# Kernel tuning notes

Measured on AMD Instinct MI355X. Metric: run time of the kernel, lower is better.

## Reference

```python
import jax, jax.numpy as jnp
import numpy as np

B, T, C, H = 8, 2048, 1024, 64

def setup_inputs() -> dict:
    key = jax.random.key(0)
    kx, kk, kq, kv = jax.random.split(key, 4)
    x = jax.random.normal(kx, (B, T, C), dtype=jnp.float32)
    # nn.Linear(n_embed, head_size, bias=False) weights stored as [C, H] (already transposed)
    s = 1.0 / np.sqrt(C)
    Wk = jax.random.normal(kk, (C, H), dtype=jnp.float32) * s
    Wq = jax.random.normal(kq, (C, H), dtype=jnp.float32) * s
    Wv = jax.random.normal(kv, (C, H), dtype=jnp.float32) * s
    return {"x": x, "Wk": Wk, "Wq": Wq, "Wv": Wv}

def reference(x, Wk, Wq, Wv):
    Bq, Tq, Cq = x.shape
    k = jnp.einsum('btc,ch->bth', x, Wk)
    q = jnp.einsum('btc,ch->bth', x, Wq)
    v = jnp.einsum('btc,ch->bth', x, Wv)
    # NOTE: faithful to source, which MULTIPLIES by C**0.5 (not 1/sqrt(head_size))
    wei = jnp.einsum('bth,bsh->bts', q, k) * (Cq ** 0.5)  # [B,T,T]
    causal = jnp.tril(jnp.ones((Tq, Tq), dtype=bool))
    wei = jnp.where(causal, wei, -jnp.inf)
    wei = jax.nn.softmax(wei, axis=-1)
    out = jnp.einsum('bts,bsh->bth', wei, v)  # [B,T,H]
    return out
```

## Files before the change

### kernel.cpp

```cpp
#include <hip/hip_runtime.h>
#include <hip/hip_bf16.h>

#define TSEQ 2048
#define CDIM 1024
#define HDIM 64
#define NROW (8 * 2048)

typedef __attribute__((ext_vector_type(8))) short bf16x8;
typedef __attribute__((ext_vector_type(4))) float f32x4;

__device__ __forceinline__ unsigned short f2bf(float f) {
    return __builtin_bit_cast(unsigned short, __float2bfloat16(f));
}
__device__ __forceinline__ float bf2f(unsigned short h) {
    unsigned int u = ((unsigned int)h) << 16;
    return __builtin_bit_cast(float, u);
}
__device__ __forceinline__ void split2(float v, unsigned short& h, unsigned short& l) {
    __hip_bfloat16 bh = __float2bfloat16(v);
    h = __builtin_bit_cast(unsigned short, bh);
    l = f2bf(v - __bfloat162float(bh));
}
__device__ __forceinline__ f32x4 mfma16(bf16x8 a, bf16x8 b, f32x4 c) {
    return __builtin_amdgcn_mfma_f32_16x16x32_bf16(a, b, c, 0, 0, 0);
}
__device__ __forceinline__ void gload_lds16(const unsigned short* g, unsigned short* l) {
    __builtin_amdgcn_global_load_lds(
        (const __attribute__((address_space(1))) unsigned int*)(g),
        (__attribute__((address_space(3))) unsigned int*)(l), 16, 0, 0);
}
__device__ __forceinline__ void gload_lds16f(const float* g, float* l) {
    __builtin_amdgcn_global_load_lds(
        (const __attribute__((address_space(1))) unsigned int*)(g),
        (__attribute__((address_space(3))) unsigned int*)(l), 16, 0, 0);
}

__global__ __launch_bounds__(256) void w_prep(
    const float* __restrict__ Wk, const float* __restrict__ Wq, const float* __restrict__ Wv,
    unsigned short* __restrict__ wThi, unsigned short* __restrict__ wTlo)
{
    __shared__ float tile[64][65];
    const int mm = blockIdx.x >> 4, kt = blockIdx.x & 15;
    const float* __restrict__ W = (mm == 0) ? Wk : (mm == 1) ? Wq : Wv;
    const int t = threadIdx.x;
    #pragma unroll
    for (int s = 0; s < 4; s++) {
        const int f = t + 256 * s;
        const int r = f >> 4, cq = f & 15;
        const float4 wv = *reinterpret_cast<const float4*>(&W[(long)(kt * 64 + r) * HDIM + 4 * cq]);
        tile[4 * cq + 0][r] = wv.x; tile[4 * cq + 1][r] = wv.y;
        tile[4 * cq + 2][r] = wv.z; tile[4 * cq + 3][r] = wv.w;
    }
    __syncthreads();
    const int n = t >> 2, seg = t & 3;
    unsigned short hi[16], lo[16];
    #pragma unroll
    for (int u = 0; u < 16; u++) split2(tile[n][16 * seg + u], hi[u], lo[u]);
    const long base = (long)(mm * 64 + n) * CDIM + kt * 64 + 16 * seg;
    *reinterpret_cast<uint4*>(&wThi[base + 0]) = *reinterpret_cast<uint4*>(&hi[0]);
    *reinterpret_cast<uint4*>(&wThi[base + 8]) = *reinterpret_cast<uint4*>(&hi[8]);
    *reinterpret_cast<uint4*>(&wTlo[base + 0]) = *reinterpret_cast<uint4*>(&lo[0]);
    *reinterpret_cast<uint4*>(&wTlo[base + 8]) = *reinterpret_cast<uint4*>(&lo[8]);
}

__global__ __launch_bounds__(512, 4) void proj_mfma(
    const float* __restrict__ x,
    const unsigned short* __restrict__ wThi, const unsigned short* __restrict__ wTlo,
    unsigned short* __restrict__ khi, unsigned short* __restrict__ klo,
    unsigned short* __restrict__ qhi, unsigned short* __restrict__ qlo,
    unsigned short* __restrict__ vt)
{
    __shared__ __align__(16) unsigned char smem[2][28672];
    const int t = threadIdx.x;
    const int lane = t & 63, w = t >> 6;
    const int r15 = lane & 15, g = lane >> 4;
    const int wr = w >> 2, wc = w & 3;
    const int bb8 = blockIdx.x & 7, jj = blockIdx.x >> 3;
    const long rowbase = (long)bb8 * TSEQ + jj * 32;

    const unsigned short* wsp[3];
    #pragma unroll
    for (int q = 0; q < 3; q++) {
        const int s = t + 512 * q;
        const int lo = (s >= 768);
        const int s7 = s - 768 * lo;
        const int row = s7 >> 2, pq = s7 & 3;
        wsp[q] = (lo ? wTlo : wThi) + (long)row * CDIM + ((pq ^ ((row >> 1) & 3)) << 3);
    }
    const int xrow_s = (t & 255) >> 3, xpq_s = t & 7;
    const float* const xsp = x + (rowbase + xrow_s) * CDIM + ((xpq_s ^ (xrow_s & 7)) << 2);

    f32x4 acc[3];
    #pragma unroll
    for (int nt = 0; nt < 3; nt++) acc[nt] = (f32x4){0.f, 0.f, 0.f, 0.f};

    auto stage = [&](int sl, int kc) {
        unsigned char* base = &smem[sl][0];
        #pragma unroll
        for (int q = 0; q < 3; q++)
            gload_lds16(wsp[q] + kc, (unsigned short*)(base + (t + 512 * q) * 16));
        if (t < 256)
            gload_lds16f(xsp + kc, (float*)(base + 24576 + t * 16));
    };

    auto compute = [&](int sl) {
        const unsigned short* wb = (const unsigned short*)&smem[sl][0];
        const float* xb = (const float*)&smem[sl][24576];
        bf16x8 ah, al;
        {
            const int rx = 16 * wr + r15;
            const int r7 = rx & 7;
            const f32x4 a0 = *reinterpret_cast<const f32x4*>(xb + rx * 32 + (((2 * g) ^ r7) << 2));
            const f32x4 a1 = *reinterpret_cast<const f32x4*>(xb + rx * 32 + (((2 * g + 1) ^ r7) << 2));
            unsigned short h0,h1,h2,h3,h4,h5,h6,h7, l0,l1,l2,l3,l4,l5,l6,l7;
            split2(a0.x, h0, l0); split2(a0.y, h1, l1); split2(a0.z, h2, l2); split2(a0.w, h3, l3);
            split2(a1.x, h4, l4); split2(a1.y, h5, l5); split2(a1.z, h6, l6); split2(a1.w, h7, l7);
            ah = (bf16x8){(short)h0,(short)h1,(short)h2,(short)h3,(short)h4,(short)h5,(short)h6,(short)h7};
            al = (bf16x8){(short)l0,(short)l1,(short)l2,(short)l3,(short)l4,(short)l5,(short)l6,(short)l7};
        }
        #pragma unroll
        for (int nt = 0; nt < 3; nt++) {
            const int rw = (3 * wc + nt) * 16 + r15;
            const int cofs = ((g ^ ((rw >> 1) & 3)) << 3);
            const bf16x8 bh = *reinterpret_cast<const bf16x8*>(wb + rw * 32 + cofs);
            const bf16x8 bl = *reinterpret_cast<const bf16x8*>(wb + 6144 + rw * 32 + cofs);
            acc[nt] = mfma16(ah, bh, acc[nt]);
            acc[nt] = mfma16(al, bh, acc[nt]);
            acc[nt] = mfma16(ah, bl, acc[nt]);
        }
    };

    stage(0, 0);
    __syncthreads();

    for (int j = 0; j < 32; ++j) {
        const int buf = j & 1;
        if (j < 31) stage(buf ^ 1, (j + 1) * 32);
        compute(buf);
        __syncthreads();
    }

    #pragma unroll
    for (int nt = 0; nt < 3; nt++) {
        const int ntg = 3 * wc + nt;
        const int mat = ntg >> 2;
        const int colin = (ntg & 3) * 16 + r15;
        const int rl = 16 * wr + 4 * g;
        if (mat == 0) {
            #pragma unroll
            for (int reg = 0; reg < 4; reg++) {
                unsigned short h, l;
                split2(acc[nt][reg], h, l);
                const long idx = (rowbase + rl + reg) * HDIM + colin;
                khi[idx] = h; klo[idx] = l;
            }
        } else if (mat == 1) {
            #pragma unroll
            for (int reg = 0; reg < 4; reg++) {
                unsigned short h, l;
                split2(acc[nt][reg] * 32.0f, h, l);
                const long idx = (rowbase + rl + reg) * HDIM + colin;
                qhi[idx] = h; qlo[idx] = l;
            }
        } else {
            ushort4 pk;
            pk.x = f2bf(acc[nt][0]); pk.y = f2bf(acc[nt][1]);
            pk.z = f2bf(acc[nt][2]); pk.w = f2bf(acc[nt][3]);
            const long idx = ((long)bb8 * 64 + colin) * TSEQ + jj * 32 + rl;
            *reinterpret_cast<ushort4*>(&vt[idx]) = pk;
        }
    }
}

__global__ __launch_bounds__(256, 2) void attn_part(
    const unsigned short* __restrict__ khi, const unsigned short* __restrict__ klo,
    const unsigned short* __restrict__ qhi, const unsigned short* __restrict__ qlo,
    const unsigned short* __restrict__ vt,
    float* __restrict__ po, float* __restrict__ pm, float* __restrict__ pl, int nsplit)
{
    __shared__ __align__(16) unsigned short ldsbuf[2][3 * 4096];
    __shared__ __align__(16) unsigned short p_lds4[4][16 * 72];
    const int t = threadIdx.x, w = t >> 6, lane = t & 63;
    const int r15 = lane & 15, g = lane >> 4;
    const int id = blockIdx.x;
    const int b = id & 7;
    const int u = id >> 3;
    const int t5 = u & 31, p = u >> 5;
    int j = (t5 & 1) ? 31 - (t5 >> 1) : (t5 >> 1);
    if (p & 1) j = 31 - j;
    const int n = j + 1;
    const int s = (p * n) / nsplit, e = ((p + 1) * n) / nsplit;
    const int pidx = (b * 32 + j) * nsplit + p;

    if (s >= e) {
        const int rr = t >> 2, cq = (t & 3) * 16;
        if ((t & 3) == 0) { pm[pidx * 64 + rr] = -3e38f; pl[pidx * 64 + rr] = 0.f; }
        const f32x4 z = (f32x4){0.f, 0.f, 0.f, 0.f};
        float* dst = &po[((long)pidx * 64 + rr) * 64 + cq];
        #pragma unroll
        for (int q = 0; q < 4; q++) *reinterpret_cast<f32x4*>(dst + 4 * q) = z;
        return;
    }

    const int row0 = t >> 3;
    const int ce = (((t & 7) ^ (row0 & 7)) << 3);
    const long bkey = (long)b * TSEQ;
    const long vrow = ((long)b * 64 + row0) * TSEQ;
    unsigned short* const lbT = &ldsbuf[0][0];

    auto stage = [&](int cur, int kb) {
        unsigned short* lb = lbT + cur * (3 * 4096) + t * 8;
        const long kgo  = (bkey + (long)kb * 64 + row0) * HDIM + ce;
        const long kgo2 = kgo + 32 * HDIM;
        const long vgo  = vrow + (long)kb * 64 + ce;
        const long vgo2 = vgo + 32L * TSEQ;
        gload_lds16(khi + kgo,  lb);
        gload_lds16(khi + kgo2, lb + 2048);
        gload_lds16(klo + kgo,  lb + 4096);
        gload_lds16(klo + kgo2, lb + 6144);
        gload_lds16(vt  + vgo,  lb + 8192);
        gload_lds16(vt  + vgo2, lb + 10240);
    };

    const long qrow = bkey + (long)j * 64 + 16 * w + r15;
    bf16x8 Qh[2], Ql[2];
    #pragma unroll
    for (int ks = 0; ks < 2; ks++) {
        Qh[ks] = *reinterpret_cast<const bf16x8*>(&qhi[qrow * HDIM + 32 * ks + 8 * g]);
        Ql[ks] = *reinterpret_cast<const bf16x8*>(&qlo[qrow * HDIM + 32 * ks + 8 * g]);
    }

    f32x4 o[4];
    #pragma unroll
    for (int ht = 0; ht < 4; ht++) o[ht] = (f32x4){0.f, 0.f, 0.f, 0.f};
    float m = -3e38f, lsum = 0.f;
    unsigned short* const pw = &p_lds4[w][0];
    const int sw = (r15 & 7) << 4;
    const int c0 = ((16 * g) ^ sw) >> 1;
    const int c1 = ((16 * g + 64) ^ sw) >> 1;

    stage(0, s);
    __syncthreads();

    for (int kb = s; kb < e; ++kb) {
        const int cur = (kb - s) & 1;
        if (kb + 1 < e) stage(cur ^ 1, kb + 1);
        const unsigned short* Kh = lbT + cur * (3 * 4096);
        const unsigned short* Kl = Kh + 4096;
        const unsigned short* Vb = Kh + 8192;
        const bool diag = (kb == j);

        f32x4 sc[4];
        #pragma unroll
        for (int mt = 0; mt < 4; mt++) {
            const bool valid = !diag || (mt <= w);
            f32x4 sv = valid ? (f32x4){0.f, 0.f, 0.f, 0.f}
                             : (f32x4){-1e30f, -1e30f, -1e30f, -1e30f};
            if (valid) {
                const int rb = (16 * mt + r15) * 64;
                const bf16x8 ah0 = *reinterpret_cast<const bf16x8*>(&Kh[rb + c0]);
                const bf16x8 ah1 = *reinterpret_cast<const bf16x8*>(&Kh[rb + c1]);
                const bf16x8 al0 = *reinterpret_cast<const bf16x8*>(&Kl[rb + c0]);
                const bf16x8 al1 = *reinterpret_cast<const bf16x8*>(&Kl[rb + c1]);
                sv = mfma16(ah0, Qh[0], sv);
                sv = mfma16(ah0, Ql[0], sv);
                sv = mfma16(al0, Qh[0], sv);
                sv = mfma16(ah1, Qh[1], sv);
                sv = mfma16(ah1, Ql[1], sv);
                sv = mfma16(al1, Qh[1], sv);
                if (diag && mt == w) {
                    #pragma unroll
                    for (int reg = 0; reg < 4; reg++)
                        if (4 * g + reg > r15) sv[reg] = -1e30f;
                }
            }
            sc[mt] = sv;
        }

        float bml = -3e38f;
        #pragma unroll
        for (int mt = 0; mt < 4; mt++)
            bml = fmaxf(bml, fmaxf(fmaxf(sc[mt][0], sc[mt][1]), fmaxf(sc[mt][2], sc[mt][3])));
        if (!__all(bml - m <= 8.0f)) {
            float bm = fmaxf(bml, __shfl_xor(bml, 16));
            bm = fmaxf(bm, __shfl_xor(bm, 32));
            const float mnew = fmaxf(m, bm);
            const float corr = __expf(m - mnew);
            lsum *= corr;
            #pragma unroll
            for (int ht = 0; ht < 4; ht++) o[ht] *= corr;
            m = mnew;
        }
        #pragma unroll
        for (int mt = 0; mt < 4; mt++) {
            const float p0 = __expf(sc[mt][0] - m);
            const float p1 = __expf(sc[mt][1] - m);
            const float p2 = __expf(sc[mt][2] - m);
            const float p3 = __expf(sc[mt][3] - m);
            lsum += (p0 + p1) + (p2 + p3);
            ushort4 pk;
            pk.x = f2bf(p0); pk.y = f2bf(p1); pk.z = f2bf(p2); pk.w = f2bf(p3);
            *reinterpret_cast<ushort4*>(&pw[r15 * 72 + 16 * mt + 4 * g]) = pk;
        }
        #pragma unroll
        for (int ks = 0; ks < 2; ks++) {
            const bf16x8 pb = *reinterpret_cast<const bf16x8*>(&pw[r15 * 72 + 32 * ks + 8 * g]);
            const int cc = ks ? c1 : c0;
            #pragma unroll
            for (int ht = 0; ht < 4; ht++) {
                const bf16x8 av = *reinterpret_cast<const bf16x8*>(&Vb[(16 * ht + r15) * 64 + cc]);
                o[ht] = mfma16(av, pb, o[ht]);
            }
        }
        __syncthreads();
    }

    lsum += __shfl_xor(lsum, 16);
    lsum += __shfl_xor(lsum, 32);
    if (g == 0) { pm[pidx * 64 + 16 * w + r15] = m; pl[pidx * 64 + 16 * w + r15] = lsum; }
    #pragma unroll
    for (int ht = 0; ht < 4; ht++)
        *reinterpret_cast<f32x4*>(&po[((long)pidx * 64 + 16 * w + r15) * 64 + 16 * ht + 4 * g]) = o[ht];
}

__global__ __launch_bounds__(256) void attn_comb(
    const float* __restrict__ po, const float* __restrict__ pm, const float* __restrict__ pl,
    float* __restrict__ out, int nsplit)
{
    const int t = threadIdx.x;
    const int b = blockIdx.x & 7, j = blockIdx.x >> 3;
    const int r = t >> 2, cq = (t & 3) * 16;
    const int base = (b * 32 + j) * nsplit;

    float M = -3e38f;
    for (int p = 0; p < nsplit; ++p) M = fmaxf(M, pm[(base + p) * 64 + r]);
    float L = 0.f;
    f32x4 acc[4];
    #pragma unroll
    for (int q = 0; q < 4; q++) acc[q] = (f32x4){0.f, 0.f, 0.f, 0.f};
    for (int p = 0; p < nsplit; ++p) {
        const float wp = __expf(pm[(base + p) * 64 + r] - M);
        L += wp * pl[(base + p) * 64 + r];
        const float* src = &po[((long)(base + p) * 64 + r) * 64 + cq];
        #pragma unroll
        for (int q = 0; q < 4; q++) acc[q] += wp * *reinterpret_cast<const f32x4*>(src + 4 * q);
    }
    const float inv = 1.0f / L;
    float* dst = &out[((long)b * TSEQ + j * 64 + r) * HDIM + cq];
    #pragma unroll
    for (int q = 0; q < 4; q++) *reinterpret_cast<f32x4*>(dst + 4 * q) = acc[q] * inv;
}

extern "C" void kernel_launch(void* const* d_in, const int* in_sizes, int n_in,
                              void* d_out, int out_size, void* d_ws, size_t ws_size,
                              hipStream_t stream) {
    const float* x  = (const float*)d_in[0];
    const float* Wk = (const float*)d_in[1];
    const float* Wq = (const float*)d_in[2];
    const float* Wv = (const float*)d_in[3];
    float* outp = (float*)d_out;

    const size_t SZ = (size_t)NROW * HDIM;
    unsigned short* ws   = (unsigned short*)d_ws;
    unsigned short* khi  = ws;
    unsigned short* klo  = ws + 1 * SZ;
    unsigned short* qhi  = ws + 2 * SZ;
    unsigned short* qlo  = ws + 3 * SZ;
    unsigned short* vt   = ws + 4 * SZ;
    unsigned short* wThi = ws + 5 * SZ;
    unsigned short* wTlo = ws + 5 * SZ + 192 * 1024;

    const size_t base_bytes = (5 * SZ + 2 * 192 * 1024) * sizeof(unsigned short);
    int nsplit = 4;
    while (nsplit > 1 && base_bytes + (size_t)nsplit * 4325376 > ws_size) nsplit >>= 1;

    float* po = (float*)((char*)d_ws + base_bytes);
    float* pm = po + (size_t)256 * 64 * 64 * nsplit;
    float* pl = pm + (size_t)256 * 64 * nsplit;

    w_prep<<<48, 256, 0, stream>>>(Wk, Wq, Wv, wThi, wTlo);
    proj_mfma<<<512, 512, 0, stream>>>(x, wThi, wTlo, khi, klo, qhi, qlo, vt);
    attn_part<<<dim3(256 * nsplit), 256, 0, stream>>>(khi, klo, qhi, qlo, vt, po, pm, pl, nsplit);
    attn_comb<<<256, 256, 0, stream>>>(po, pm, pl, outp, nsplit);
}
```

Measured before the change: 73.19 us.

## Pre-split x into bf16 hi/lo and use larger-tile projection kernel

```diff
diff --git a/kernel.cpp b/kernel.cpp
--- a/kernel.cpp
+++ b/kernel.cpp
@@ -61,6 +61,144 @@
     *reinterpret_cast<uint4*>(&wThi[base + 8]) = *reinterpret_cast<uint4*>(&hi[8]);
     *reinterpret_cast<uint4*>(&wTlo[base + 0]) = *reinterpret_cast<uint4*>(&lo[0]);
     *reinterpret_cast<uint4*>(&wTlo[base + 8]) = *reinterpret_cast<uint4*>(&lo[8]);
+}
+
+__global__ __launch_bounds__(256) void x_prep(
+    const float* __restrict__ x,
+    unsigned short* __restrict__ xhi, unsigned short* __restrict__ xlo)
+{
+    const long base = (long)blockIdx.x * 2048;
+    const int t = threadIdx.x;
+    #pragma unroll
+    for (int i = 0; i < 8; i++) {
+        const long f4 = base + t + 256 * i;
+        const float4 v = reinterpret_cast<const float4*>(x)[f4];
+        ushort4 h, l;
+        split2(v.x, h.x, l.x); split2(v.y, h.y, l.y);
+        split2(v.z, h.z, l.z); split2(v.w, h.w, l.w);
+        reinterpret_cast<ushort4*>(xhi)[f4] = h;
+        reinterpret_cast<ushort4*>(xlo)[f4] = l;
+    }
+}
+
+__global__ __launch_bounds__(512, 1) void proj_mfma2(
+    const unsigned short* __restrict__ xhi, const unsigned short* __restrict__ xlo,
+    const unsigned short* __restrict__ wThi, const unsigned short* __restrict__ wTlo,
+    unsigned short* __restrict__ khi, unsigned short* __restrict__ klo,
+    unsigned short* __restrict__ qhi, unsigned short* __restrict__ qlo,
+    unsigned short* __restrict__ vt)
+{
+    extern __shared__ __align__(16) unsigned short smem2[];
+    const int t = threadIdx.x;
+    const int lane = t & 63, w = t >> 6;
+    const int r15 = lane & 15, g = lane >> 4;
+    const int wr = w >> 2, wc = w & 3;
+    const int bb8 = blockIdx.x & 7, jj = blockIdx.x >> 3;
+    const long rowbase = (long)bb8 * TSEQ + jj * 64;
+
+    long wsrc[3];
+    #pragma unroll
+    for (int q = 0; q < 3; q++) {
+        const int s = t + 512 * q;
+        const int row = s >> 3, gr = s & 7;
+        wsrc[q] = (long)row * CDIM + ((gr ^ (row & 7)) << 3);
+    }
+    const int xr = t >> 3, xg = t & 7;
+    const long xsrc = (rowbase + xr) * CDIM + ((xg ^ (xr & 7)) << 3);
+
+    f32x4 acc[2][3];
+    #pragma unroll
+    for (int mt = 0; mt < 2; mt++)
+        #pragma unroll
+        for (int nt = 0; nt < 3; nt++) acc[mt][nt] = (f32x4){0.f, 0.f, 0.f, 0.f};
+
+    auto stage = [&](int buf, int kc) {
+        unsigned short* b = smem2 + buf * 32768;
+        #pragma unroll
+        for (int q = 0; q < 3; q++) {
+            gload_lds16(wThi + wsrc[q] + kc, b + (t + 512 * q) * 8);
+            gload_lds16(wTlo + wsrc[q] + kc, b + 12288 + (t + 512 * q) * 8);
+        }
+        gload_lds16(xhi + xsrc + kc, b + 24576 + t * 8);
+        gload_lds16(xlo + xsrc + kc, b + 28672 + t * 8);
+    };
+
+    auto compute = [&](int buf) {
+        const unsigned short* b = smem2 + buf * 32768;
+        const unsigned short* Wh = b, *Wl = b + 12288, *Xh = b + 24576, *Xl = b + 28672;
+        bf16x8 ah[2][2], al[2][2];
+        #pragma unroll
+        for (int mt = 0; mt < 2; mt++) {
+            const int rx = 32 * wr + 16 * mt + r15;
+            const int r7 = rx & 7;
+            #pragma unroll
+            for (int ks = 0; ks < 2; ks++) {
+                const int go = ((4 * ks + g) ^ r7) << 3;
+                ah[mt][ks] = *reinterpret_cast<const bf16x8*>(Xh + rx * 64 + go);
+                al[mt][ks] = *reinterpret_cast<const bf16x8*>(Xl + rx * 64 + go);
+            }
+        }
+        #pragma unroll
+        for (int nt = 0; nt < 3; nt++) {
+            const int rw = (3 * wc + nt) * 16 + r15;
+            const int r7w = rw & 7;
+            #pragma unroll
+            for (int ks = 0; ks < 2; ks++) {
+                const int go = ((4 * ks + g) ^ r7w) << 3;
+                const bf16x8 bh = *reinterpret_cast<const bf16x8*>(Wh + rw * 64 + go);
+                const bf16x8 bl = *reinterpret_cast<const bf16x8*>(Wl + rw * 64 + go);
+                #pragma unroll
+                for (int mt = 0; mt < 2; mt++) {
+                    acc[mt][nt] = mfma16(ah[mt][ks], bh, acc[mt][nt]);
+                    acc[mt][nt] = mfma16(al[mt][ks], bh, acc[mt][nt]);
+                    acc[mt][nt] = mfma16(ah[mt][ks], bl, acc[mt][nt]);
+                }
+            }
+        }
+    };
+
+    stage(0, 0);
+    __syncthreads();
+    for (int j = 0; j < 16; ++j) {
+        const int buf = j & 1;
+        if (j < 15) stage(buf ^ 1, (j + 1) * 64);
+        compute(buf);
+        __syncthreads();
+    }
+
+    #pragma unroll
+    for (int nt = 0; nt < 3; nt++) {
+        const int ntg = 3 * wc + nt;
+        const int mat = ntg >> 2;
+        const int colin = (ntg & 3) * 16 + r15;
+        #pragma unroll
+        for (int mt = 0; mt < 2; mt++) {
+            const int rl = 32 * wr + 16 * mt + 4 * g;
+            if (mat == 0) {
+                #pragma unroll
+                for (int reg = 0; reg < 4; reg++) {
+                    unsigned short h, l;
+                    split2(acc[mt][nt][reg], h, l);
+                    const long idx = (rowbase + rl + reg) * HDIM + colin;
+                    khi[idx] = h; klo[idx] = l;
+                }
+            } else if (mat == 1) {
+                #pragma unroll
+                for (int reg = 0; reg < 4; reg++) {
+                    unsigned short h, l;
+                    split2(acc[mt][nt][reg] * 32.0f, h, l);
+                    const long idx = (rowbase + rl + reg) * HDIM + colin;
+                    qhi[idx] = h; qlo[idx] = l;
+                }
+            } else {
+                ushort4 pk;
+                pk.x = f2bf(acc[mt][nt][0]); pk.y = f2bf(acc[mt][nt][1]);
+                pk.z = f2bf(acc[mt][nt][2]); pk.w = f2bf(acc[mt][nt][3]);
+                const long idx = ((long)bb8 * 64 + colin) * TSEQ + jj * 64 + rl;
+                *reinterpret_cast<ushort4*>(&vt[idx]) = pk;
+            }
+        }
+    }
 }
 
 __global__ __launch_bounds__(512, 4) void proj_mfma(
@@ -102,7 +240,6 @@
         if (t < 256)
             gload_lds16f(xsp + kc, (float*)(base + 24576 + t * 16));
     };
-
     auto compute = [&](int sl) {
         const unsigned short* wb = (const unsigned short*)&smem[sl][0];
         const float* xb = (const float*)&smem[sl][24576];
@@ -132,7 +269,6 @@
 
     stage(0, 0);
     __syncthreads();
-
     for (int j = 0; j < 32; ++j) {
         const int buf = j & 1;
         if (j < 31) stage(buf ^ 1, (j + 1) * 32);
@@ -370,16 +506,28 @@
     unsigned short* wThi = ws + 5 * SZ;
     unsigned short* wTlo = ws + 5 * SZ + 192 * 1024;
 
-    const size_t base_bytes = (5 * SZ + 2 * 192 * 1024) * sizeof(unsigned short);
+    const size_t base_b   = (5 * SZ + 2 * 192 * 1024) * 2;
+    const size_t xsplit_b = (size_t)2 * NROW * CDIM * 2;
+    const size_t per_split = 4325376;
+
+    const bool prep = (ws_size >= base_b + xsplit_b + per_split);
     int nsplit = 4;
-    while (nsplit > 1 && base_bytes + (size_t)nsplit * 4325376 > ws_size) nsplit >>= 1;
-
-    float* po = (float*)((char*)d_ws + base_bytes);
+    const size_t fixed = base_b + (prep ? xsplit_b : 0);
+    while (nsplit > 1 && fixed + (size_t)nsplit * per_split > ws_size) nsplit >>= 1;
+
+    unsigned short* xhi = ws + base_b / 2;
+    unsigned short* xlo = xhi + (size_t)NROW * CDIM;
+    float* po = (float*)((char*)d_ws + fixed);
     float* pm = po + (size_t)256 * 64 * 64 * nsplit;
     float* pl = pm + (size_t)256 * 64 * nsplit;
 
     w_prep<<<48, 256, 0, stream>>>(Wk, Wq, Wv, wThi, wTlo);
-    proj_mfma<<<512, 512, 0, stream>>>(x, wThi, wTlo, khi, klo, qhi, qlo, vt);
+    if (prep) {
+        x_prep<<<2048, 256, 0, stream>>>(x, xhi, xlo);
+        proj_mfma2<<<256, 512, 131072, stream>>>(xhi, xlo, wThi, wTlo, khi, klo, qhi, qlo, vt);
+    } else {
+        proj_mfma<<<512, 512, 0, stream>>>(x, wThi, wTlo, khi, klo, qhi, qlo, vt);
+    }
     attn_part<<<dim3(256 * nsplit), 256, 0, stream>>>(khi, klo, qhi, qlo, vt, po, pm, pl, nsplit);
     attn_comb<<<256, 256, 0, stream>>>(po, pm, pl, outp, nsplit);
 }
```

After: 84.35 us. 15.3% more time.
